# Optimization experiments

Measured on AMD Instinct MI355X. Metric: run time of the kernel, lower is better.

The kernel has to match this reference:

```python
import jax, jax.numpy as jnp
import numpy as np

B, C, H, W = 8, 256, 64, 64
NUM_HEADS, N_WIN, TOPK = 8, 8, 4
MLP_RATIO = 3


def setup_inputs() -> dict:
    key = jax.random.key(0)
    ks = jax.random.split(key, 8)
    rn = lambda k, shp, s=0.02: jax.random.normal(k, shp, dtype=jnp.float32) * s
    return {
        "x": jax.random.normal(ks[0], (B, C, H, W), dtype=jnp.float32),
        "pos_w": rn(ks[1], (C, 1, 3, 3)),
        "pos_b": jnp.zeros((C,), jnp.float32),
        "ln1_g": jnp.ones((C,), jnp.float32),
        "ln1_b": jnp.zeros((C,), jnp.float32),
        "qkv_w": rn(ks[2], (3 * C, C)),
        "qkv_b": jnp.zeros((3 * C,), jnp.float32),
        "lepe_w": rn(ks[3], (C, 1, 5, 5)),
        "lepe_b": jnp.zeros((C,), jnp.float32),
        "out_w": rn(ks[4], (C, C)),
        "out_b": jnp.zeros((C,), jnp.float32),
        "ln2_g": jnp.ones((C,), jnp.float32),
        "ln2_b": jnp.zeros((C,), jnp.float32),
        "mlp_w1": rn(ks[5], (C, MLP_RATIO * C)),
        "mlp_b1": jnp.zeros((MLP_RATIO * C,), jnp.float32),
        "mlp_w2": rn(ks[6], (MLP_RATIO * C, C)),
        "mlp_b2": jnp.zeros((C,), jnp.float32),
    }


def _dwconv(x, w, b, pad):
    # depthwise conv, x NCHW, w [C,1,k,k]
    y = jax.lax.conv_general_dilated(x, w, (1, 1), [(pad, pad), (pad, pad)],
        dimension_numbers=("NCHW", "OIHW", "NCHW"), feature_group_count=x.shape[1])
    return y + b[None, :, None, None]


def _conv1x1(x, w, b):
    return jnp.einsum("nchw,oc->nohw", x, w) + b[None, :, None, None]


def _ln(x, g, b, eps=1e-6):
    mu = x.mean(-1, keepdims=True)
    var = ((x - mu) ** 2).mean(-1, keepdims=True)
    return (x - mu) * jax.lax.rsqrt(var + eps) * g + b


def _grid2seq(x, rs, m):
    Bb, Cc, Hh, Ww = x.shape
    rh, rw = Hh // rs[0], Ww // rs[1]
    d = Cc // m
    x = x.reshape(Bb, m, d, rh, rs[0], rw, rs[1])
    x = x.transpose(0, 1, 3, 5, 4, 6, 2)  # b m rh rw p q d
    return x.reshape(Bb, m, rh * rw, rs[0] * rs[1], d), rh, rw


def _seq2grid(x, rh, rw, rs):
    Bb, m, nr, rsq, d = x.shape
    x = x.reshape(Bb, m, rh, rw, rs[0], rs[1], d)
    x = x.transpose(0, 1, 6, 2, 4, 3, 5)  # b m d rh p rw q
    return x.reshape(Bb, m * d, rh * rs[0], rw * rs[1])


def _dssa(x, qkv_w, qkv_b, lepe_w, lepe_b, out_w, out_b):
    # x: NHWC -> NCHW
    x = x.transpose(0, 3, 1, 2)
    Nn, Cc, Hh, Ww = x.shape
    rs = (Hh // N_WIN, Ww // N_WIN)
    scale = Cc ** -0.5  # DSSA uses dim**-0.5
    qkv = _conv1x1(x, qkv_w, qkv_b)
    q, k, v = jnp.split(qkv, 3, axis=1)
    # routing (detached in the original)
    qd, kd = jax.lax.stop_gradient(q), jax.lax.stop_gradient(k)
    q_r = qd.reshape(Nn, Cc, N_WIN, rs[0], N_WIN, rs[1]).mean(axis=(3, 5))
    k_r = kd.reshape(Nn, Cc, N_WIN, rs[0], N_WIN, rs[1]).mean(axis=(3, 5))
    q_r = q_r.reshape(Nn, Cc, -1).transpose(0, 2, 1)   # [N, nr, C]
    k_r = k_r.reshape(Nn, Cc, -1)                      # [N, C, nr]
    a_r = q_r @ k_r                                    # [N, nr, nr]
    _, idx = jax.lax.top_k(a_r, TOPK)                  # [N, nr, topk]
    qs, rh, rw = _grid2seq(q, rs, NUM_HEADS)           # [N,m,nr,rsq,d]
    ks_, _, _ = _grid2seq(k, rs, NUM_HEADS)
    vs, _, _ = _grid2seq(v, rs, NUM_HEADS)
    gather = jax.vmap(lambda t, ii: t[:, ii])          # per-batch region gather
    key_g = gather(ks_, idx)                           # [N,m,nr,topk,rsq,d]
    val_g = gather(vs, idx)
    Nn_, m_, nr, rsq, d = qs.shape
    key_g = key_g.reshape(Nn, m_, nr, TOPK * rsq, d)
    val_g = val_g.reshape(Nn, m_, nr, TOPK * rsq, d)
    attn = jnp.einsum("bmrqd,bmrkd->bmrqk", qs * scale, key_g)  # [N,m,nr,rsq,topk*rsq]
    k2 = TOPK * rsq // 8
    score, index = jax.lax.top_k(attn, k2)             # [N,m,nr,rsq,k2]
    v_sel = jnp.take_along_axis(val_g[:, :, :, None, :, :], index[..., None], axis=4)
    a = jax.nn.softmax(score, axis=-1)
    out = jnp.einsum("bmrqk,bmrqkd->bmrqd", a, v_sel)
    out = _seq2grid(out, rh, rw, rs)                   # NCHW
    out = out + _dwconv(v, lepe_w, lepe_b, 2)
    out = _conv1x1(out, out_w, out_b)
    return out.transpose(0, 2, 3, 1)                   # NHWC


def reference(x, pos_w, pos_b, ln1_g, ln1_b, qkv_w, qkv_b, lepe_w, lepe_b,
              out_w, out_b, ln2_g, ln2_b, mlp_w1, mlp_b1, mlp_w2, mlp_b2):
    x = x + _dwconv(x, pos_w, pos_b, 1)
    x = x.transpose(0, 2, 3, 1)  # NHWC
    x = x + _dssa(_ln(x, ln1_g, ln1_b), qkv_w, qkv_b, lepe_w, lepe_b, out_w, out_b)
    h = _ln(x, ln2_g, ln2_b)
    h = jax.nn.gelu(h @ mlp_w1 + mlp_b1, approximate=False)
    x = x + (h @ mlp_w2 + mlp_b2)
    return x.transpose(0, 3, 1, 2)  # NCHW
```

## Files before the change

### kernel.cpp

```cpp
#include <hip/hip_runtime.h>
#include <cmath>


typedef __bf16 bf16x8 __attribute__((ext_vector_type(8)));
typedef __bf16 bf16x4 __attribute__((ext_vector_type(4)));
typedef float f32x4 __attribute__((ext_vector_type(4)));
typedef float f32x2 __attribute__((ext_vector_type(2)));
typedef unsigned short us4 __attribute__((ext_vector_type(4)));

__device__ __forceinline__ void async_copy16(const __bf16* g, __bf16* l) {
  __builtin_amdgcn_global_load_lds(
      (const __attribute__((address_space(1))) void*)g,
      (__attribute__((address_space(3))) void*)l, 16, 0, 0);
}

__global__ __launch_bounds__(256) void transpose_kernel(
    const float* __restrict__ src, float* __restrict__ dst, int R, int Cc) {
  __shared__ float T[64][65];
  int b = blockIdx.z;
  int r0 = blockIdx.y * 64, c0 = blockIdx.x * 64;
  const float* S = src + (size_t)b * R * Cc;
  float* D = dst + (size_t)b * R * Cc;
  int lane = threadIdx.x & 63, wq = threadIdx.x >> 6;
#pragma unroll
  for (int j = 0; j < 16; j++) {
    int rr = wq + j * 4;
    T[rr][lane] = S[(size_t)(r0 + rr) * Cc + c0 + lane];
  }
  __syncthreads();
#pragma unroll
  for (int j = 0; j < 16; j++) {
    int cc = wq + j * 4;
    D[(size_t)(c0 + cc) * R + r0 + lane] = T[lane][cc];
  }
}

__global__ __launch_bounds__(256) void posconv_kernel(
    const float* __restrict__ xt, const float* __restrict__ pw,
    const float* __restrict__ pb, float* __restrict__ xa) {
  __shared__ float Ls[100][64];
  __shared__ float Ws[9][64];
  int blk = blockIdx.x;
  int b = blk >> 8, r = (blk >> 2) & 63, cg = blk & 3;
  int h0 = (r >> 3) << 3, w0 = (r & 7) << 3;
  int c0 = cg << 6;
  int tid = threadIdx.x, cl = tid & 63;
  const float* src = xt + ((size_t)b * 4096) * 256;
  for (int i = tid; i < 6400; i += 256) {
    int pos = i >> 6, ccl = i & 63;
    int hh = h0 + (pos / 10) - 1, ww = w0 + (pos % 10) - 1;
    float val = 0.f;
    if (hh >= 0 && hh < 64 && ww >= 0 && ww < 64)
      val = src[(size_t)(hh * 64 + ww) * 256 + c0 + ccl];
    Ls[pos][ccl] = val;
  }
  for (int i = tid; i < 576; i += 256) {
    int tap = i >> 6, ccl = i & 63;
    Ws[tap][ccl] = pw[(c0 + ccl) * 9 + tap];
  }
  __syncthreads();
  float bias = pb[c0 + cl];
  for (int j = 0; j < 16; j++) {
    int p = (tid >> 6) + (j << 2);
    int ph = p >> 3, pww = p & 7;
    float acc = bias;
#pragma unroll
    for (int dh = 0; dh < 3; dh++)
#pragma unroll
      for (int dw = 0; dw < 3; dw++)
        acc += Ls[(ph + dh) * 10 + (pww + dw)][cl] * Ws[dh * 3 + dw][cl];
    float xv = Ls[(ph + 1) * 10 + (pww + 1)][cl];
    xa[((size_t)(b * 4096 + (h0 + ph) * 64 + (w0 + pww))) * 256 + c0 + cl] =
        xv + acc;
  }
}

__global__ __launch_bounds__(256) void ln1mean_kernel(
    const float* __restrict__ xa, const float* __restrict__ g,
    const float* __restrict__ bb, __bf16* __restrict__ lnb,
    float* __restrict__ lnm) {
  __shared__ float part[4][256];
  int blk = blockIdx.x;
  int b = blk >> 6, r = blk & 63;
  int h0 = (r >> 3) << 3, w0 = (r & 7) << 3;
  int wave = threadIdx.x >> 6, l = threadIdx.x & 63;
  float ga = g[l], gb2 = g[l + 64], gc = g[l + 128], gd = g[l + 192];
  float ba = bb[l], bb2 = bb[l + 64], bc = bb[l + 128], bd = bb[l + 192];
  float a0 = 0.f, a1 = 0.f, a2 = 0.f, a3 = 0.f;
  for (int t = 0; t < 16; t++) {
    int p = wave * 16 + t;
    int h = h0 + (p >> 3), w = w0 + (p & 7);
    size_t tok = (size_t)(b * 4096 + h * 64 + w) * 256;
    const float* row = xa + tok;
    float v0 = row[l], v1 = row[l + 64], v2 = row[l + 128], v3 = row[l + 192];
    float s = v0 + v1 + v2 + v3;
#pragma unroll
    for (int off = 32; off; off >>= 1) s += __shfl_xor(s, off);
    float mu = s * (1.f / 256.f);
    float d0 = v0 - mu, d1 = v1 - mu, d2 = v2 - mu, d3 = v3 - mu;
    float sq = d0 * d0 + d1 * d1 + d2 * d2 + d3 * d3;
#pragma unroll
    for (int off = 32; off; off >>= 1) sq += __shfl_xor(sq, off);
    float rstd = rsqrtf(sq * (1.f / 256.f) + 1e-6f);
    float n0 = d0 * rstd, n1 = d1 * rstd, n2 = d2 * rstd, n3 = d3 * rstd;
    __bf16* o = lnb + tok;
    o[l]       = (__bf16)(n0 * ga + ba);
    o[l + 64]  = (__bf16)(n1 * gb2 + bb2);
    o[l + 128] = (__bf16)(n2 * gc + bc);
    o[l + 192] = (__bf16)(n3 * gd + bd);
    a0 += n0; a1 += n1; a2 += n2; a3 += n3;
  }
  part[wave][l] = a0; part[wave][l + 64] = a1;
  part[wave][l + 128] = a2; part[wave][l + 192] = a3;
  __syncthreads();
  if (wave == 0) {
    for (int ch = l; ch < 256; ch += 64) {
      float s2 = part[0][ch] + part[1][ch] + part[2][ch] + part[3][ch];
      lnm[(size_t)(b * 64 + r) * 256 + ch] = g[ch] * (s2 * (1.f / 64.f)) + bb[ch];
    }
  }
}

__global__ __launch_bounds__(256) void wprep_kernel(
    const float* __restrict__ qkv_w, const float* __restrict__ out_w,
    const float* __restrict__ w1, const float* __restrict__ w2,
    __bf16* __restrict__ wq, __bf16* __restrict__ wo,
    __bf16* __restrict__ w1t, __bf16* __restrict__ w2t) {
  int i = blockIdx.x * 256 + threadIdx.x;
  if (i < 196608) wq[i] = (__bf16)qkv_w[i];
  if (i < 65536) wo[i] = (__bf16)out_w[i];
  if (i < 196608) {
    int n = i >> 8, k2 = i & 255;
    w1t[i] = (__bf16)w1[k2 * 768 + n];
  }
  if (i < 196608) {
    int n = i / 768, k2 = i % 768;
    w2t[i] = (__bf16)w2[k2 * 256 + n];
  }
}

template <int EPI>
__global__ __launch_bounds__(256) void mfma_gemm(
    const __bf16* __restrict__ A, const __bf16* __restrict__ Bw,
    const float* __restrict__ bias, const float* __restrict__ res,
    float* __restrict__ out, __bf16* __restrict__ outb,
    __bf16* __restrict__ qd, __bf16* __restrict__ kd, __bf16* __restrict__ vd,
    int N, int K, int row0) {
  __shared__ __bf16 Asl[128 * 32];
  __shared__ __bf16 Bsl[128 * 32];
  int tid = threadIdx.x;
  int lane = tid & 63, wave = tid >> 6;
  int m0 = blockIdx.y * 128, n0 = blockIdx.x * 128;
  int wr = (wave >> 1) * 64, wc = (wave & 1) * 64;

  f32x4 acc[4][4];
  f32x4 z = {0.f, 0.f, 0.f, 0.f};
#pragma unroll
  for (int i = 0; i < 4; i++)
#pragma unroll
    for (int j = 0; j < 4; j++) acc[i][j] = z;

  int srow = (lane >> 2);
  int skoff = (lane & 3) * 8;
  for (int k0 = 0; k0 < K; k0 += 32) {
#pragma unroll
    for (int j = 0; j < 2; j++) {
      int rbase = wave * 32 + j * 16;
      const __bf16* ga = A + (size_t)(m0 + rbase + srow) * K + k0 + skoff;
      const __bf16* gb = Bw + (size_t)(n0 + rbase + srow) * K + k0 + skoff;
      async_copy16(ga, &Asl[rbase * 32]);
      async_copy16(gb, &Bsl[rbase * 32]);
    }
    __syncthreads();
    bf16x8 af[4], bf[4];
#pragma unroll
    for (int t = 0; t < 4; t++) {
      af[t] = *(const bf16x8*)&Asl[(wr + t * 16 + (lane & 15)) * 32 + (lane >> 4) * 8];
      bf[t] = *(const bf16x8*)&Bsl[(wc + t * 16 + (lane & 15)) * 32 + (lane >> 4) * 8];
    }
#pragma unroll
    for (int ti = 0; ti < 4; ti++)
#pragma unroll
      for (int tj = 0; tj < 4; tj++)
        acc[ti][tj] = __builtin_amdgcn_mfma_f32_16x16x32_bf16(
            af[ti], bf[tj], acc[ti][tj], 0, 0, 0);
    __syncthreads();
  }
#pragma unroll
  for (int ti = 0; ti < 4; ti++) {
#pragma unroll
    for (int tj = 0; tj < 4; tj++) {
      int colg = n0 + wc + tj * 16 + (lane & 15);
      float bv = bias[colg];
#pragma unroll
      for (int reg = 0; reg < 4; reg++) {
        int rowg = m0 + wr + ti * 16 + (lane >> 4) * 4 + reg;
        float val = acc[ti][tj][reg] + bv;
        if (EPI == 0) {
          int tns = colg >> 8, cc = colg & 255, m = cc >> 5, d = cc & 31;
          int grow = row0 + rowg;
          int b = grow >> 12, hw = grow & 4095, h = hw >> 6, w = hw & 63;
          int r = ((h >> 3) << 3) | (w >> 3), s2 = ((h & 7) << 3) | (w & 7);
          size_t addr = (size_t)(b * 8 + m) * 131072 + r * 2048 + s2 * 32 + d;
          if (tns == 0) qd[addr] = (__bf16)(val * 0.0625f);
          else if (tns == 1) kd[addr] = (__bf16)val;
          else vd[addr] = (__bf16)val;
        } else if (EPI == 2) {
          outb[(size_t)rowg * N + colg] =
              (__bf16)(0.5f * val * (1.f + erff(val * 0.70710678118654752f)));
        } else {
          int grow = row0 + rowg;
          int b = grow >> 12, hw = grow & 4095;
          out[(size_t)(b * 256 + colg) * 4096 + hw] =
              res[(size_t)grow * 256 + colg] + val;
        }
      }
    }
  }
}

__global__ __launch_bounds__(512) void gemm_ln_kernel(
    const __bf16* A, const __bf16* __restrict__ Bw,
    const float* __restrict__ bias, float* __restrict__ xa,
    const float* __restrict__ g2, const float* __restrict__ b2,
    __bf16* lnbo) {
  __shared__ __bf16 Asl[128 * 32];
  __shared__ __bf16 Bsl[256 * 32];
  __shared__ float part1[128][4];
  __shared__ float part2[128][4];
  __shared__ float muv[128];
  __shared__ float rsv[128];
  int tid = threadIdx.x;
  int lane = tid & 63, wave = tid >> 6;
  int m0 = blockIdx.x * 128;
  int wr = (wave >> 2) * 64, wc = (wave & 3) * 64;

  f32x4 acc[4][4];
  f32x4 z = {0.f, 0.f, 0.f, 0.f};
#pragma unroll
  for (int i = 0; i < 4; i++)
#pragma unroll
    for (int j = 0; j < 4; j++) acc[i][j] = z;

  int srow = lane >> 2, skoff = (lane & 3) * 8;
  for (int k0 = 0; k0 < 256; k0 += 32) {
#pragma unroll
    for (int j = 0; j < 3; j++) {
      int seg = wave + 8 * j;
      if (seg < 8) {
        const __bf16* ga = A + (size_t)(m0 + seg * 16 + srow) * 256 + k0 + skoff;
        async_copy16(ga, &Asl[seg * 16 * 32]);
      } else {
        const __bf16* gb =
            Bw + (size_t)((seg - 8) * 16 + srow) * 256 + k0 + skoff;
        async_copy16(gb, &Bsl[(seg - 8) * 16 * 32]);
      }
    }
    __syncthreads();
    bf16x8 af[4], bf[4];
#pragma unroll
    for (int t = 0; t < 4; t++) {
      af[t] = *(const bf16x8*)&Asl[(wr + t * 16 + (lane & 15)) * 32 + (lane >> 4) * 8];
      bf[t] = *(const bf16x8*)&Bsl[(wc + t * 16 + (lane & 15)) * 32 + (lane >> 4) * 8];
    }
#pragma unroll
    for (int ti = 0; ti < 4; ti++)
#pragma unroll
      for (int tj = 0; tj < 4; tj++)
        acc[ti][tj] = __builtin_amdgcn_mfma_f32_16x16x32_bf16(
            af[ti], bf[tj], acc[ti][tj], 0, 0, 0);
    __syncthreads();
  }

  float s1[16], s2v[16];
#pragma unroll
  for (int k = 0; k < 16; k++) { s1[k] = 0.f; s2v[k] = 0.f; }
#pragma unroll
  for (int tj = 0; tj < 4; tj++) {
    int colg = wc + tj * 16 + (lane & 15);
    float bv = bias[colg];
#pragma unroll
    for (int ti = 0; ti < 4; ti++) {
#pragma unroll
      for (int reg = 0; reg < 4; reg++) {
        int rowg = m0 + wr + ti * 16 + (lane >> 4) * 4 + reg;
        float v = acc[ti][tj][reg] + bv + xa[(size_t)rowg * 256 + colg];
        xa[(size_t)rowg * 256 + colg] = v;
        acc[ti][tj][reg] = v;
        s1[ti * 4 + reg] += v;
        s2v[ti * 4 + reg] += v * v;
      }
    }
  }
#pragma unroll
  for (int off = 1; off < 16; off <<= 1) {
#pragma unroll
    for (int k = 0; k < 16; k++) {
      s1[k] += __shfl_xor(s1[k], off);
      s2v[k] += __shfl_xor(s2v[k], off);
    }
  }
  if ((lane & 15) == 0) {
    int q = lane >> 4;
#pragma unroll
    for (int k = 0; k < 16; k++) {
      int rowl = wr + (k >> 2) * 16 + q * 4 + (k & 3);
      part1[rowl][wave & 3] = s1[k];
      part2[rowl][wave & 3] = s2v[k];
    }
  }
  __syncthreads();
  if (tid < 128) {
    float S1 = part1[tid][0] + part1[tid][1] + part1[tid][2] + part1[tid][3];
    float S2 = part2[tid][0] + part2[tid][1] + part2[tid][2] + part2[tid][3];
    float mu = S1 * (1.f / 256.f);
    float var = S2 * (1.f / 256.f) - mu * mu;
    muv[tid] = mu;
    rsv[tid] = rsqrtf(var + 1e-6f);
  }
  __syncthreads();
#pragma unroll
  for (int tj = 0; tj < 4; tj++) {
    int colg = wc + tj * 16 + (lane & 15);
    float gg = g2[colg], bb = b2[colg];
#pragma unroll
    for (int ti = 0; ti < 4; ti++) {
#pragma unroll
      for (int reg = 0; reg < 4; reg++) {
        int rowl = wr + ti * 16 + (lane >> 4) * 4 + reg;
        int rowg = m0 + rowl;
        lnbo[(size_t)rowg * 256 + colg] =
            (__bf16)((acc[ti][tj][reg] - muv[rowl]) * rsv[rowl] * gg + bb);
      }
    }
  }
}

__global__ __launch_bounds__(256) void qkr_kernel(
    const float* __restrict__ lnm, const float* __restrict__ qkv_w,
    const float* __restrict__ qkv_b, float* __restrict__ qr,
    float* __restrict__ kr) {
  __shared__ float xm[256];
  int br = blockIdx.x, c = threadIdx.x;
  xm[c] = lnm[(size_t)br * 256 + c];
  __syncthreads();
  const float* wqp = qkv_w + (size_t)c * 256;
  const float* wkp = qkv_w + (size_t)(256 + c) * 256;
  float aq = 0.f, ak = 0.f;
  for (int k2 = 0; k2 < 256; k2++) {
    float xv = xm[k2];
    aq += wqp[k2] * xv; ak += wkp[k2] * xv;
  }
  qr[(size_t)br * 256 + c] = aq + qkv_b[c];
  kr[(size_t)br * 256 + c] = ak + qkv_b[256 + c];
}

__global__ __launch_bounds__(256) void routing_kernel(
    const float* __restrict__ qr, const float* __restrict__ kr,
    int* __restrict__ idxout) {
  __shared__ float Ar[4][64];
  int b = blockIdx.y, rg = blockIdx.x;
  int tid = threadIdx.x;
  int lane = tid & 63, wave = tid >> 6;
  int i = (rg << 2) + wave;
  const float* qrow = qr + (size_t)(b * 64 + i) * 256;
  const float* krow = kr + (size_t)(b * 64 + lane) * 256;
  float acc = 0.f;
  for (int c = 0; c < 256; c++) acc += qrow[c] * krow[c];
  Ar[wave][lane] = acc;
  __syncthreads();
  if (lane == 0) {
    float v0 = -INFINITY, v1 = -INFINITY, v2 = -INFINITY, v3 = -INFINITY;
    int i0 = 0, i1 = 0, i2 = 0, i3 = 0;
    for (int j = 0; j < 64; j++) {
      float s = Ar[wave][j];
      if (s > v0)      { v3=v2;i3=i2; v2=v1;i2=i1; v1=v0;i1=i0; v0=s;i0=j; }
      else if (s > v1) { v3=v2;i3=i2; v2=v1;i2=i1; v1=s;i1=j; }
      else if (s > v2) { v3=v2;i3=i2; v2=s;i2=j; }
      else if (s > v3) { v3=s;i3=j; }
    }
    int* op = idxout + (b * 64 + i) * 4;
    op[0] = i0; op[1] = i1; op[2] = i2; op[3] = i3;
  }
}

__global__ __launch_bounds__(256, 4) void attn_kernel(
    const __bf16* __restrict__ qbf, float* __restrict__ aout,
    const __bf16* __restrict__ kbuf, const __bf16* __restrict__ vbuf,
    const int* __restrict__ idx) {
  __shared__ __bf16 Vt[32 * 256];
  __shared__ __bf16 Sb[32 * 256];
  __shared__ float wsum_l[32];
  int blk = blockIdx.x; int r = blk & 63; int m = (blk >> 6) & 7; int b = blk >> 9;
  int tid = threadIdx.x;
  int lane = tid & 63, wave = tid >> 6;
  const int* ip = idx + (b * 64 + r) * 4;
  size_t bm = (size_t)(b * 8 + m) * 131072;
  int rgs[4] = {ip[0], ip[1], ip[2], ip[3]};

  {
    int s = tid >> 2, g8 = tid & 3;
#pragma unroll
    for (int t = 0; t < 4; t++) {
      const uint4* sv = (const uint4*)(vbuf + bm + (size_t)rgs[t] * 2048);
      uint4 vw = sv[tid];
      int kk = (t << 6) | s;
      int ck = kk >> 3, klo = kk & 7;
      union { uint4 u; __bf16 h[8]; } vu; vu.u = vw;
#pragma unroll
      for (int j = 0; j < 8; j++) {
        int d = (g8 << 3) + j;
        int cp = (ck + j + (g8 << 1)) & 31;
        Vt[(d << 8) + (cp << 3) + klo] = vu.h[j];
      }
    }
  }

  const __bf16* qb = qbf + bm + r * 2048;
  bf16x8 qf[4];
#pragma unroll
  for (int rt = 0; rt < 4; rt++)
    qf[rt] = *(const bf16x8*)(qb + ((rt * 16 + (lane & 15)) << 5) + ((lane >> 4) << 3));

  bf16x8 kf[4];
  {
    int rw0 = (wave & 1) ? rgs[1] : rgs[0];
    int rw1 = (wave & 1) ? rgs[3] : rgs[2];
    int rgw = (wave & 2) ? rw1 : rw0;
    const __bf16* kb = kbuf + bm + (size_t)rgw * 2048;
#pragma unroll
    for (int kt4 = 0; kt4 < 4; kt4++)
      kf[kt4] = *(const bf16x8*)(kb + ((kt4 * 16 + (lane & 15)) << 5) + ((lane >> 4) << 3));
  }

#pragma unroll
  for (int c = 0; c < 2; c++) {
#pragma unroll
    for (int kt4 = 0; kt4 < 4; kt4++) {
      int kt = (wave << 2) + kt4;
#pragma unroll
      for (int rt = 0; rt < 2; rt++) {
        f32x4 st = {0.f, 0.f, 0.f, 0.f};
        st = __builtin_amdgcn_mfma_f32_16x16x32_bf16(kf[kt4], qf[(c << 1) | rt],
                                                     st, 0, 0, 0);
        int row = (rt << 4) + (lane & 15);
        int key0 = (kt << 4) + ((lane >> 4) << 2);
        bf16x4 sv4;
#pragma unroll
        for (int j = 0; j < 4; j++) sv4[j] = (__bf16)st[j];
        *(bf16x4*)&Sb[row * 256 + (key0 ^ ((row & 7) << 3))] = sv4;
      }
    }
    __syncthreads();

    {
      int row0 = wave << 3;
      unsigned uk[8][4];
#pragma unroll
      for (int i = 0; i < 8; i++) {
        us4 q4 = *(const us4*)&Sb[(row0 + i) * 256 + ((lane << 2) ^ (i << 3))];
#pragma unroll
        for (int t = 0; t < 4; t++) {
          unsigned bits = q4[t];
          uk[i][t] = (bits ^ ((0u - (bits >> 15)) | 0x8000u)) & 0xFFFFu;
        }
      }
      unsigned p[8];
#pragma unroll
      for (int i = 0; i < 8; i++) p[i] = 0;
      for (int bit = 15; bit >= 0; --bit) {
        unsigned msk = 1u << bit;
#pragma unroll
        for (int i = 0; i < 8; i++) {
          unsigned cc = p[i] | msk;
          int n = __popcll(__ballot(uk[i][0] >= cc)) + __popcll(__ballot(uk[i][1] >= cc)) +
                  __popcll(__ballot(uk[i][2] >= cc)) + __popcll(__ballot(uk[i][3] >= cc));
          if (n >= 32) p[i] = cc;
        }
      }
#pragma unroll
      for (int i = 0; i < 8; i++) {
        unsigned T = p[i];
        unsigned ub = T << 16;
        unsigned tb = (ub & 0x80000000u) ? (ub ^ 0x80000000u) : ~ub;
        float Tv = __uint_as_float(tb);
        unsigned long long gbb[4], ebb[4];
#pragma unroll
        for (int t = 0; t < 4; t++) {
          gbb[t] = __ballot(uk[i][t] > T);
          ebb[t] = __ballot(uk[i][t] == T);
        }
        int cgt = __popcll(gbb[0]) + __popcll(gbb[1]) + __popcll(gbb[2]) + __popcll(gbb[3]);
        int be1 = __popcll(ebb[0]), be2 = be1 + __popcll(ebb[1]), be3 = be2 + __popcll(ebb[2]);
        int bes[4] = {0, be1, be2, be3};
        int need = 32 - cgt;
        bf16x4 pq;
        float part = 0.f;
#pragma unroll
        for (int t = 0; t < 4; t++) {
          int ret = bes[t] + __builtin_amdgcn_mbcnt_hi(
                                 (unsigned)(ebb[t] >> 32),
                                 __builtin_amdgcn_mbcnt_lo((unsigned)ebb[t], 0));
          bool isg = uk[i][t] > T;
          bool sel = isg || (uk[i][t] == T && ret < need);
          unsigned bits = uk[i][t] ^ ((uk[i][t] >> 15) ? 0x8000u : 0xFFFFu);
          float scv = __uint_as_float(bits << 16);
          float w = sel ? __expf(scv - Tv) : 0.f;
          __bf16 wb = (__bf16)w;
          pq[t] = wb;
          part += (float)wb;
        }
        *(bf16x4*)&Sb[(row0 + i) * 256 + ((lane << 2) ^ (i << 3))] = pq;
#pragma unroll
        for (int off = 32; off; off >>= 1) part += __shfl_xor(part, off);
        if (lane == 0) wsum_l[row0 + i] = part;
      }
    }
    __syncthreads();

    f32x4 oacc = {0.f, 0.f, 0.f, 0.f};
    int prow = ((wave >> 1) << 4) + (lane & 15);
    int drow = ((wave & 1) << 4) + (lane & 15);
    int koff = (lane >> 4) << 3;
#pragma unroll
    for (int ks = 0; ks < 8; ks++) {
      bf16x8 pa = *(const bf16x8*)&Sb[prow * 256 + (((ks << 5) + koff) ^ ((prow & 7) << 3))];
      int ck = (ks << 2) + (lane >> 4);
      int cp = (ck + (drow & 7) + ((drow >> 3) << 1)) & 31;
      bf16x8 vb = *(const bf16x8*)&Vt[(drow << 8) + (cp << 3)];
      oacc = __builtin_amdgcn_mfma_f32_16x16x32_bf16(pa, vb, oacc, 0, 0, 0);
    }
    {
      int rl = ((wave >> 1) << 4) + ((lane >> 4) << 2);
      float* ob = aout + bm + r * 2048;
#pragma unroll
      for (int reg = 0; reg < 4; reg++) {
        float rinv = __builtin_amdgcn_rcpf(wsum_l[rl + reg]);
        int rowg = (c << 5) + rl + reg;
        ob[(rowg << 5) + ((wave & 1) << 4) + (lane & 15)] = oacc[reg] * rinv;
      }
    }
    __syncthreads();
  }
}

__global__ __launch_bounds__(256) void lepe_kernel(
    const float* __restrict__ ao, const __bf16* __restrict__ v,
    const float* __restrict__ lw, const float* __restrict__ lb,
    __bf16* __restrict__ tout) {
  __shared__ float Ls[144][32];
  __shared__ float Ws[25][32];
  int blk = blockIdx.x;
  int b = blk >> 9, m = (blk >> 6) & 7, r = blk & 63;
  int h0 = (r >> 3) << 3, w0 = (r & 7) << 3;
  int tid = threadIdx.x, d = tid & 31;
  size_t bm = (size_t)(b * 8 + m) * 131072;
  for (int i = tid; i < 144 * 32; i += 256) {
    int pos = i >> 5, dd = i & 31;
    int hh = h0 + (pos / 12) - 2, ww = w0 + (pos % 12) - 2;
    float val = 0.f;
    if (hh >= 0 && hh < 64 && ww >= 0 && ww < 64) {
      int r2 = ((hh >> 3) << 3) | (ww >> 3), s2 = ((hh & 7) << 3) | (ww & 7);
      val = (float)v[bm + r2 * 2048 + s2 * 32 + dd];
    }
    Ls[pos][dd] = val;
  }
  for (int i = tid; i < 800; i += 256) {
    int tap = i >> 5, dd = i & 31;
    Ws[tap][dd] = lw[(m * 32 + dd) * 25 + tap];
  }
  __syncthreads();
  int c = m * 32 + d;
  float bias = lb[c];
  for (int j = 0; j < 8; j++) {
    int p = (tid >> 5) + (j << 3);
    int ph = p >> 3, pww = p & 7;
    float acc = bias;
#pragma unroll
    for (int dh = 0; dh < 5; dh++)
#pragma unroll
      for (int dw = 0; dw < 5; dw++)
        acc += Ls[(ph + dh) * 12 + (pww + dw)][d] * Ws[dh * 5 + dw][d];
    acc += ao[bm + r * 2048 + p * 32 + d];
    tout[((size_t)(b * 4096 + (h0 + ph) * 64 + (w0 + pww))) * 256 + c] =
        (__bf16)acc;
  }
}

extern "C" void kernel_launch(void* const* d_in, const int* in_sizes, int n_in,
                              void* d_out, int out_size, void* d_ws, size_t ws_size,
                              hipStream_t stream) {
  (void)in_sizes; (void)n_in; (void)out_size; (void)ws_size;
  const float* x      = (const float*)d_in[0];
  const float* pos_w  = (const float*)d_in[1];
  const float* pos_b  = (const float*)d_in[2];
  const float* ln1_g  = (const float*)d_in[3];
  const float* ln1_b  = (const float*)d_in[4];
  const float* qkv_w  = (const float*)d_in[5];
  const float* qkv_b  = (const float*)d_in[6];
  const float* lepe_w = (const float*)d_in[7];
  const float* lepe_b = (const float*)d_in[8];
  const float* out_w  = (const float*)d_in[9];
  const float* out_b  = (const float*)d_in[10];
  const float* ln2_g  = (const float*)d_in[11];
  const float* ln2_b  = (const float*)d_in[12];
  const float* mlp_w1 = (const float*)d_in[13];
  const float* mlp_b1 = (const float*)d_in[14];
  const float* mlp_w2 = (const float*)d_in[15];
  const float* mlp_b2 = (const float*)d_in[16];

  float* ws = (float*)d_ws;
  const size_t P = 8ull * 4096 * 256;
  size_t off = 0;
  float* xa = ws + off; off += P;
  float* q  = ws + off; off += P;
  __bf16* k = (__bf16*)(ws + off); off += P / 2;
  __bf16* v = (__bf16*)(ws + off); off += P / 2;
  __bf16* lnb = (__bf16*)(ws + off); off += P / 2;
  __bf16* hb  = (__bf16*)(ws + off); off += 12582912;
  __bf16* wq  = (__bf16*)(ws + off); off += 98304;
  __bf16* wo  = (__bf16*)(ws + off); off += 32768;
  __bf16* w1t = (__bf16*)(ws + off); off += 98304;
  __bf16* w2t = (__bf16*)(ws + off); off += 98304;
  float* qr  = ws + off; off += 131072;
  float* kr  = ws + off; off += 131072;
  float* lnm = ws + off; off += 131072;
  int* ridx  = (int*)(ws + off);

  __bf16* qbf = hb;

  wprep_kernel<<<768, 256, 0, stream>>>(qkv_w, out_w, mlp_w1, mlp_w2,
                                        wq, wo, w1t, w2t);
  transpose_kernel<<<dim3(64, 4, 8), 256, 0, stream>>>(x, q, 256, 4096);
  posconv_kernel<<<2048, 256, 0, stream>>>(q, pos_w, pos_b, xa);
  ln1mean_kernel<<<512, 256, 0, stream>>>(xa, ln1_g, ln1_b, lnb, lnm);
  qkr_kernel<<<512, 256, 0, stream>>>(lnm, qkv_w, qkv_b, qr, kr);
  routing_kernel<<<dim3(16, 8), 256, 0, stream>>>(qr, kr, ridx);
  mfma_gemm<0><<<dim3(6, 256), 256, 0, stream>>>(
      lnb, wq, qkv_b, nullptr, nullptr, nullptr, qbf, k, v, 768, 256, 0);
  attn_kernel<<<4096, 256, 0, stream>>>(qbf, q, k, v, ridx);
  lepe_kernel<<<4096, 256, 0, stream>>>(q, v, lepe_w, lepe_b, lnb);
  gemm_ln_kernel<<<256, 512, 0, stream>>>(lnb, wo, out_b, xa, ln2_g, ln2_b,
                                          lnb);
  mfma_gemm<2><<<dim3(6, 256), 256, 0, stream>>>(
      lnb, w1t, mlp_b1, nullptr, nullptr, hb, nullptr, nullptr, nullptr,
      768, 256, 0);
  mfma_gemm<3><<<dim3(2, 256), 256, 0, stream>>>(
      hb, w2t, mlp_b2, xa, (float*)d_out, nullptr, nullptr, nullptr, nullptr,
      256, 768, 0);
}
```

Baseline: 552.2 us.

## Process both query chunks in parallel with 512-thread attention blocks

The attention kernel used to loop over two 32-row query chunks with 4 waves, synchronizing between stages. It now launches 8 waves per block so each half handles one chunk concurrently. This removes the serial chunk loop and one round of barriers, and splits the V tile load across the extra threads. In exchange it doubles the score buffer in shared memory to 48KB per block, which may limit how many blocks fit on a compute unit.

Measured after the change: 540.2 us. 2.2% less time.

```diff
diff --git a/kernel.cpp b/kernel.cpp
--- a/kernel.cpp
+++ b/kernel.cpp
@@ -384,13 +384,13 @@
   }
 }
 
-__global__ __launch_bounds__(256, 4) void attn_kernel(
+__global__ __launch_bounds__(512, 6) void attn_kernel(
     const __bf16* __restrict__ qbf, float* __restrict__ aout,
     const __bf16* __restrict__ kbuf, const __bf16* __restrict__ vbuf,
     const int* __restrict__ idx) {
   __shared__ __bf16 Vt[32 * 256];
-  __shared__ __bf16 Sb[32 * 256];
-  __shared__ float wsum_l[32];
+  __shared__ __bf16 Sb[64 * 256];
+  __shared__ float wsum_l[64];
   int blk = blockIdx.x; int r = blk & 63; int m = (blk >> 6) & 7; int b = blk >> 9;
   int tid = threadIdx.x;
   int lane = tid & 63, wave = tid >> 6;
@@ -399,12 +399,18 @@
   int rgs[4] = {ip[0], ip[1], ip[2], ip[3]};
 
   {
-    int s = tid >> 2, g8 = tid & 3;
-#pragma unroll
-    for (int t = 0; t < 4; t++) {
-      const uint4* sv = (const uint4*)(vbuf + bm + (size_t)rgs[t] * 2048);
-      uint4 vw = sv[tid];
-      int kk = (t << 6) | s;
+    int tid2 = tid & 255;
+    int rid = tid >> 8;
+    int s = tid2 >> 2, g8 = tid2 & 3;
+#pragma unroll
+    for (int t = 0; t < 2; t++) {
+      int rgi = (t << 1) | rid;
+      int rlo = (rgi & 1) ? rgs[1] : rgs[0];
+      int rhi = (rgi & 1) ? rgs[3] : rgs[2];
+      int rgv = (rgi & 2) ? rhi : rlo;
+      const uint4* sv = (const uint4*)(vbuf + bm + (size_t)rgv * 2048);
+      uint4 vw = sv[tid2];
+      int kk = (rgi << 6) | s;
       int ck = kk >> 3, klo = kk & 7;
       union { uint4 u; __bf16 h[8]; } vu; vu.u = vw;
 #pragma unroll
@@ -416,11 +422,14 @@
     }
   }
 
+  int chnk = wave >> 2;
   const __bf16* qb = qbf + bm + r * 2048;
-  bf16x8 qf[4];
-#pragma unroll
-  for (int rt = 0; rt < 4; rt++)
-    qf[rt] = *(const bf16x8*)(qb + ((rt * 16 + (lane & 15)) << 5) + ((lane >> 4) << 3));
+  bf16x8 qf[2];
+#pragma unroll
+  for (int rtl = 0; rtl < 2; rtl++) {
+    int rt = (chnk << 1) + rtl;
+    qf[rtl] = *(const bf16x8*)(qb + ((rt * 16 + (lane & 15)) << 5) + ((lane >> 4) << 3));
+  }
 
   bf16x8 kf[4];
   {
@@ -434,113 +443,108 @@
   }
 
 #pragma unroll
-  for (int c = 0; c < 2; c++) {
-#pragma unroll
-    for (int kt4 = 0; kt4 < 4; kt4++) {
-      int kt = (wave << 2) + kt4;
-#pragma unroll
-      for (int rt = 0; rt < 2; rt++) {
-        f32x4 st = {0.f, 0.f, 0.f, 0.f};
-        st = __builtin_amdgcn_mfma_f32_16x16x32_bf16(kf[kt4], qf[(c << 1) | rt],
-                                                     st, 0, 0, 0);
-        int row = (rt << 4) + (lane & 15);
-        int key0 = (kt << 4) + ((lane >> 4) << 2);
-        bf16x4 sv4;
-#pragma unroll
-        for (int j = 0; j < 4; j++) sv4[j] = (__bf16)st[j];
-        *(bf16x4*)&Sb[row * 256 + (key0 ^ ((row & 7) << 3))] = sv4;
-      }
-    }
-    __syncthreads();
-
-    {
-      int row0 = wave << 3;
-      unsigned uk[8][4];
+  for (int kt4 = 0; kt4 < 4; kt4++) {
+    int kt = ((wave & 3) << 2) + kt4;
+#pragma unroll
+    for (int rtl = 0; rtl < 2; rtl++) {
+      f32x4 st = {0.f, 0.f, 0.f, 0.f};
+      st = __builtin_amdgcn_mfma_f32_16x16x32_bf16(kf[kt4], qf[rtl], st, 0, 0, 0);
+      int row = (chnk << 5) + (rtl << 4) + (lane & 15);
+      int key0 = (kt << 4) + ((lane >> 4) << 2);
+      bf16x4 sv4;
+#pragma unroll
+      for (int j = 0; j < 4; j++) sv4[j] = (__bf16)st[j];
+      *(bf16x4*)&Sb[row * 256 + (key0 ^ ((row & 7) << 3))] = sv4;
+    }
+  }
+  __syncthreads();
+
+  {
+    int row0 = wave << 3;
+    unsigned uk[8][4];
+#pragma unroll
+    for (int i = 0; i < 8; i++) {
+      us4 q4 = *(const us4*)&Sb[(row0 + i) * 256 + ((lane << 2) ^ (i << 3))];
+#pragma unroll
+      for (int t = 0; t < 4; t++) {
+        unsigned bits = q4[t];
+        uk[i][t] = (bits ^ ((0u - (bits >> 15)) | 0x8000u)) & 0xFFFFu;
+      }
+    }
+    unsigned p[8];
+#pragma unroll
+    for (int i = 0; i < 8; i++) p[i] = 0;
+    for (int bit = 15; bit >= 0; --bit) {
+      unsigned msk = 1u << bit;
 #pragma unroll
       for (int i = 0; i < 8; i++) {
-        us4 q4 = *(const us4*)&Sb[(row0 + i) * 256 + ((lane << 2) ^ (i << 3))];
-#pragma unroll
-        for (int t = 0; t < 4; t++) {
-          unsigned bits = q4[t];
-          uk[i][t] = (bits ^ ((0u - (bits >> 15)) | 0x8000u)) & 0xFFFFu;
-        }
-      }
-      unsigned p[8];
-#pragma unroll
-      for (int i = 0; i < 8; i++) p[i] = 0;
-      for (int bit = 15; bit >= 0; --bit) {
-        unsigned msk = 1u << bit;
-#pragma unroll
-        for (int i = 0; i < 8; i++) {
-          unsigned cc = p[i] | msk;
-          int n = __popcll(__ballot(uk[i][0] >= cc)) + __popcll(__ballot(uk[i][1] >= cc)) +
-                  __popcll(__ballot(uk[i][2] >= cc)) + __popcll(__ballot(uk[i][3] >= cc));
-          if (n >= 32) p[i] = cc;
-        }
-      }
-#pragma unroll
-      for (int i = 0; i < 8; i++) {
-        unsigned T = p[i];
-        unsigned ub = T << 16;
-        unsigned tb = (ub & 0x80000000u) ? (ub ^ 0x80000000u) : ~ub;
-        float Tv = __uint_as_float(tb);
-        unsigned long long gbb[4], ebb[4];
-#pragma unroll
-        for (int t = 0; t < 4; t++) {
-          gbb[t] = __ballot(uk[i][t] > T);
-          ebb[t] = __ballot(uk[i][t] == T);
-        }
-        int cgt = __popcll(gbb[0]) + __popcll(gbb[1]) + __popcll(gbb[2]) + __popcll(gbb[3]);
-        int be1 = __popcll(ebb[0]), be2 = be1 + __popcll(ebb[1]), be3 = be2 + __popcll(ebb[2]);
-        int bes[4] = {0, be1, be2, be3};
-        int need = 32 - cgt;
-        bf16x4 pq;
-        float part = 0.f;
-#pragma unroll
-        for (int t = 0; t < 4; t++) {
-          int ret = bes[t] + __builtin_amdgcn_mbcnt_hi(
-                                 (unsigned)(ebb[t] >> 32),
-                                 __builtin_amdgcn_mbcnt_lo((unsigned)ebb[t], 0));
-          bool isg = uk[i][t] > T;
-          bool sel = isg || (uk[i][t] == T && ret < need);
-          unsigned bits = uk[i][t] ^ ((uk[i][t] >> 15) ? 0x8000u : 0xFFFFu);
-          float scv = __uint_as_float(bits << 16);
-          float w = sel ? __expf(scv - Tv) : 0.f;
-          __bf16 wb = (__bf16)w;
-          pq[t] = wb;
-          part += (float)wb;
-        }
-        *(bf16x4*)&Sb[(row0 + i) * 256 + ((lane << 2) ^ (i << 3))] = pq;
-#pragma unroll
-        for (int off = 32; off; off >>= 1) part += __shfl_xor(part, off);
-        if (lane == 0) wsum_l[row0 + i] = part;
-      }
-    }
-    __syncthreads();
-
-    f32x4 oacc = {0.f, 0.f, 0.f, 0.f};
-    int prow = ((wave >> 1) << 4) + (lane & 15);
-    int drow = ((wave & 1) << 4) + (lane & 15);
-    int koff = (lane >> 4) << 3;
-#pragma unroll
-    for (int ks = 0; ks < 8; ks++) {
-      bf16x8 pa = *(const bf16x8*)&Sb[prow * 256 + (((ks << 5) + koff) ^ ((prow & 7) << 3))];
-      int ck = (ks << 2) + (lane >> 4);
-      int cp = (ck + (drow & 7) + ((drow >> 3) << 1)) & 31;
-      bf16x8 vb = *(const bf16x8*)&Vt[(drow << 8) + (cp << 3)];
-      oacc = __builtin_amdgcn_mfma_f32_16x16x32_bf16(pa, vb, oacc, 0, 0, 0);
-    }
-    {
-      int rl = ((wave >> 1) << 4) + ((lane >> 4) << 2);
-      float* ob = aout + bm + r * 2048;
-#pragma unroll
-      for (int reg = 0; reg < 4; reg++) {
-        float rinv = __builtin_amdgcn_rcpf(wsum_l[rl + reg]);
-        int rowg = (c << 5) + rl + reg;
-        ob[(rowg << 5) + ((wave & 1) << 4) + (lane & 15)] = oacc[reg] * rinv;
-      }
-    }
-    __syncthreads();
+        unsigned cc = p[i] | msk;
+        int n = __popcll(__ballot(uk[i][0] >= cc)) + __popcll(__ballot(uk[i][1] >= cc)) +
+                __popcll(__ballot(uk[i][2] >= cc)) + __popcll(__ballot(uk[i][3] >= cc));
+        if (n >= 32) p[i] = cc;
+      }
+    }
+#pragma unroll
+    for (int i = 0; i < 8; i++) {
+      unsigned T = p[i];
+      unsigned ub = T << 16;
+      unsigned tb = (ub & 0x80000000u) ? (ub ^ 0x80000000u) : ~ub;
+      float Tv = __uint_as_float(tb);
+      unsigned long long gbb[4], ebb[4];
+#pragma unroll
+      for (int t = 0; t < 4; t++) {
+        gbb[t] = __ballot(uk[i][t] > T);
+        ebb[t] = __ballot(uk[i][t] == T);
+      }
+      int cgt = __popcll(gbb[0]) + __popcll(gbb[1]) + __popcll(gbb[2]) + __popcll(gbb[3]);
+      int be1 = __popcll(ebb[0]), be2 = be1 + __popcll(ebb[1]), be3 = be2 + __popcll(ebb[2]);
+      int bes[4] = {0, be1, be2, be3};
+      int need = 32 - cgt;
+      bf16x4 pq;
+      float part = 0.f;
+#pragma unroll
+      for (int t = 0; t < 4; t++) {
+        int ret = bes[t] + __builtin_amdgcn_mbcnt_hi(
+                               (unsigned)(ebb[t] >> 32),
+                               __builtin_amdgcn_mbcnt_lo((unsigned)ebb[t], 0));
+        bool isg = uk[i][t] > T;
+        bool sel = isg || (uk[i][t] == T && ret < need);
+        unsigned bits = uk[i][t] ^ ((uk[i][t] >> 15) ? 0x8000u : 0xFFFFu);
+        float scv = __uint_as_float(bits << 16);
+        float w = sel ? __expf(scv - Tv) : 0.f;
+        __bf16 wb = (__bf16)w;
+        pq[t] = wb;
+        part += (float)wb;
+      }
+      *(bf16x4*)&Sb[(row0 + i) * 256 + ((lane << 2) ^ (i << 3))] = pq;
+#pragma unroll
+      for (int off = 32; off; off >>= 1) part += __shfl_xor(part, off);
+      if (lane == 0) wsum_l[row0 + i] = part;
+    }
+  }
+  __syncthreads();
+
+  f32x4 oacc = {0.f, 0.f, 0.f, 0.f};
+  int prow = ((wave >> 1) << 4) + (lane & 15);
+  int drow = ((wave & 1) << 4) + (lane & 15);
+  int koff = (lane >> 4) << 3;
+#pragma unroll
+  for (int ks = 0; ks < 8; ks++) {
+    bf16x8 pa = *(const bf16x8*)&Sb[prow * 256 + (((ks << 5) + koff) ^ ((prow & 7) << 3))];
+    int ck = (ks << 2) + (lane >> 4);
+    int cp = (ck + (drow & 7) + ((drow >> 3) << 1)) & 31;
+    bf16x8 vb = *(const bf16x8*)&Vt[(drow << 8) + (cp << 3)];
+    oacc = __builtin_amdgcn_mfma_f32_16x16x32_bf16(pa, vb, oacc, 0, 0, 0);
+  }
+  {
+    int rl = ((wave >> 1) << 4) + ((lane >> 4) << 2);
+    float* ob = aout + bm + r * 2048;
+#pragma unroll
+    for (int reg = 0; reg < 4; reg++) {
+      float rinv = __builtin_amdgcn_rcpf(wsum_l[rl + reg]);
+      int rowg = rl + reg;
+      ob[(rowg << 5) + ((wave & 1) << 4) + (lane & 15)] = oacc[reg] * rinv;
+    }
   }
 }
 
@@ -638,7 +642,7 @@
   routing_kernel<<<dim3(16, 8), 256, 0, stream>>>(qr, kr, ridx);
   mfma_gemm<0><<<dim3(6, 256), 256, 0, stream>>>(
       lnb, wq, qkv_b, nullptr, nullptr, nullptr, qbf, k, v, 768, 256, 0);
-  attn_kernel<<<4096, 256, 0, stream>>>(qbf, q, k, v, ridx);
+  attn_kernel<<<4096, 512, 0, stream>>>(qbf, q, k, v, ridx);
   lepe_kernel<<<4096, 256, 0, stream>>>(q, v, lepe_w, lepe_b, lnb);
   gemm_ln_kernel<<<256, 512, 0, stream>>>(lnb, wo, out_b, xa, ln2_g, ln2_b,
                                           lnb);
```
